# Kernel tuning notes

Hardware: AMD Instinct MI355X
Metric: run time of the kernel (lower is better)

Reference implementation:

```python
import jax, jax.numpy as jnp
import numpy as np

B, S, D, H, F = 2, 1024, 2048, 16, 8192
DH = D // H
MAX_ALPHA = 0.2
CN_SCALE = D / (D - 1)  # CenterNorm scale factor dim/(dim-1)


def setup_inputs() -> dict:
    key = jax.random.key(0)
    ks = jax.random.split(key, 8)
    s = 0.02
    f32 = jnp.float32
    return {
        "x": jax.random.normal(ks[0], (B, S, D), f32),
        "ln1_g": jnp.ones((D,), f32), "ln1_b": jnp.zeros((D,), f32),
        "wq": jax.random.normal(ks[1], (D, D), f32) * s, "bq": jnp.zeros((D,), f32),
        "wk": jax.random.normal(ks[2], (D, D), f32) * s, "bk": jnp.zeros((D,), f32),
        "wv": jax.random.normal(ks[3], (D, D), f32) * s, "bv": jnp.zeros((D,), f32),
        "wo": jax.random.normal(ks[4], (D, D), f32) * s, "bo": jnp.zeros((D,), f32),
        "tau": jnp.ones((H,), f32),   # learnable per-head temperature, init_tau=1.0
        "nu": jnp.ones((H,), f32),    # learnable per-head output scale, init_nu=1.0
        "alpha1": jnp.full((D,), 0.1, f32),  # per-channel residual weight, init 0.1
        "ln2_g": jnp.ones((D,), f32), "ln2_b": jnp.zeros((D,), f32),
        "w1": jax.random.normal(ks[5], (F, D), f32) * s, "b1": jnp.zeros((F,), f32),
        "w2": jax.random.normal(ks[6], (D, F), f32) * s, "b2": jnp.zeros((D,), f32),
        "alpha2": jnp.full((D,), 0.1, f32),
    }


def _center_norm(x, g, b):
    # CenterNorm: subtract mean only (no variance), scale by dim/(dim-1)
    mu = jnp.mean(x, axis=-1, keepdims=True)
    return g * (CN_SCALE * (x - mu)) + b


def _l2norm(t):
    return t / (jnp.linalg.norm(t, axis=-1, keepdims=True) + 1e-6)


def _cosine_attn(x, wq, bq, wk, bk, wv, bv, wo, bo, tau, nu):
    # project and split heads -> [B,H,S,DH]
    def proj(w, b):
        return (jnp.einsum('bsd,ed->bse', x, w) + b).reshape(B, S, H, DH).transpose(0, 2, 1, 3)
    q, k, v = proj(wq, bq), proj(wk, bk), proj(wv, bv)
    qn, kn = _l2norm(q), _l2norm(k)  # cosine similarity attention
    scores = jnp.einsum('bhqd,bhkd->bhqk', qn, kn) * tau[None, :, None, None]
    causal = jnp.tril(jnp.ones((S, S), bool))
    scores = jnp.where(causal[None, None], scores, -jnp.inf)
    p = jax.nn.softmax(scores, axis=-1)
    o = jnp.einsum('bhqk,bhkd->bhqd', p, v) * nu[None, :, None, None]
    o = o.transpose(0, 2, 1, 3).reshape(B, S, D)
    return jnp.einsum('bsd,ed->bse', o, wo) + bo


def _ffn(x, w1, b1, w2, b2):
    h = jax.nn.gelu(jnp.einsum('bsd,fd->bsf', x, w1) + b1)
    return jnp.einsum('bsf,df->bsd', h, w2) + b2


def reference(x, ln1_g, ln1_b, wq, bq, wk, bk, wv, bv, wo, bo, tau, nu,
              alpha1, ln2_g, ln2_b, w1, b1, w2, b2, alpha2):
    a = _center_norm(x, ln1_g, ln1_b)
    a1 = jnp.clip(alpha1, -MAX_ALPHA, MAX_ALPHA)
    x1 = a + a1 * _cosine_attn(a, wq, bq, wk, bk, wv, bv, wo, bo, tau, nu)
    m = _center_norm(x1, ln2_g, ln2_b)
    a2 = jnp.clip(alpha2, -MAX_ALPHA, MAX_ALPHA)
    return m + a2 * _ffn(m, w1, b1, w2, b2)
```

## Files before the change

### kernel.cpp

```cpp
#include <hip/hip_runtime.h>
#include <hip/hip_bf16.h>
#include <stdint.h>

#define B_ 2
#define S_ 1024
#define D_ 2048
#define H_ 16
#define F_ 8192
#define DH_ 128
#define M_ 2048

typedef unsigned short u16;
typedef __attribute__((ext_vector_type(8))) short short8;
typedef __attribute__((ext_vector_type(4))) float f32x4;
typedef __attribute__((ext_vector_type(2))) float f32x2;

__device__ __forceinline__ u16 f2bf(float f) {
  union { float f; uint32_t u; } c; c.f = f;
  uint32_t r = c.u + 0x7FFFu + ((c.u >> 16) & 1u);
  return (u16)(r >> 16);
}

__device__ __forceinline__ float bf2f(u16 v) {
  union { uint32_t u; float f; } c; c.u = ((uint32_t)v) << 16;
  return c.f;
}

__device__ __forceinline__ void gload16(const void* g, void* l) {
  __builtin_amdgcn_global_load_lds((const __attribute__((address_space(1))) void*)g,
                                   (__attribute__((address_space(3))) void*)l, 16, 0, 0);
}

__device__ __forceinline__ float clipa(float a) {
  return fminf(0.2f, fmaxf(-0.2f, a));
}

__device__ __forceinline__ float gelu_f(float x) {
  float z = 0.7978845608028654f * (x + 0.044715f * x * x * x);
  z = fminf(10.f, fmaxf(-10.f, z));
  float e = __expf(2.f * z);
  return 0.5f * x * (1.f + (e - 1.f) / (e + 1.f));
}

__global__ __launch_bounds__(256) void k_cvt_all(const float* __restrict__ wq,
                                                 const float* __restrict__ wk,
                                                 const float* __restrict__ wv,
                                                 const float* __restrict__ wo,
                                                 const float* __restrict__ w1,
                                                 const float* __restrict__ w2,
                                                 u16* __restrict__ dst) {
  const int tot = 6291456;
  for (int gi = blockIdx.x * 256 + threadIdx.x; gi < tot; gi += 2048 * 256) {
    const float* s;
    int off;
    if (gi < 2097152) {
      int r = gi >> 19;
      s = r == 0 ? wq : (r == 1 ? wk : (r == 2 ? wv : wo));
      off = gi & 524287;
    } else if (gi < 4194304) {
      s = w1; off = gi - 2097152;
    } else {
      s = w2; off = gi - 4194304;
    }
    f32x4 a = *(const f32x4*)(s + (size_t)off * 8);
    f32x4 b = *(const f32x4*)(s + (size_t)off * 8 + 4);
    short8 o;
    o[0] = (short)f2bf(a[0]); o[1] = (short)f2bf(a[1]);
    o[2] = (short)f2bf(a[2]); o[3] = (short)f2bf(a[3]);
    o[4] = (short)f2bf(b[0]); o[5] = (short)f2bf(b[1]);
    o[6] = (short)f2bf(b[2]); o[7] = (short)f2bf(b[3]);
    *(short8*)(dst + (size_t)gi * 8) = o;
  }
}

__global__ __launch_bounds__(256) void k_centernorm(const float* __restrict__ x,
                                                    const float* __restrict__ g,
                                                    const float* __restrict__ bb,
                                                    float* __restrict__ of,
                                                    u16* __restrict__ ob) {
  const int row = blockIdx.x;
  const int t = threadIdx.x;
  const float* xr = x + (size_t)row * D_;
  f32x4 v0 = *(const f32x4*)(xr + t * 8);
  f32x4 v1 = *(const f32x4*)(xr + t * 8 + 4);
  float s = v0[0] + v0[1] + v0[2] + v0[3] + v1[0] + v1[1] + v1[2] + v1[3];
#pragma unroll
  for (int off = 1; off < 64; off <<= 1) s += __shfl_xor(s, off);
  __shared__ float red[4];
  if ((t & 63) == 0) red[t >> 6] = s;
  __syncthreads();
  const float mu = (red[0] + red[1] + red[2] + red[3]) * (1.0f / D_);
  const float CNS = (float)D_ / (float)(D_ - 1);
  f32x4 g0 = *(const f32x4*)(g + t * 8);
  f32x4 g1 = *(const f32x4*)(g + t * 8 + 4);
  f32x4 b0 = *(const f32x4*)(bb + t * 8);
  f32x4 b1 = *(const f32x4*)(bb + t * 8 + 4);
  f32x4 y0, y1;
  short8 yb;
#pragma unroll
  for (int i = 0; i < 4; i++) {
    y0[i] = g0[i] * (CNS * (v0[i] - mu)) + b0[i];
    y1[i] = g1[i] * (CNS * (v1[i] - mu)) + b1[i];
  }
#pragma unroll
  for (int i = 0; i < 4; i++) { yb[i] = (short)f2bf(y0[i]); yb[4 + i] = (short)f2bf(y1[i]); }
  float* orow = of + (size_t)row * D_;
  *(f32x4*)(orow + t * 8) = y0;
  *(f32x4*)(orow + t * 8 + 4) = y1;
  *(short8*)(ob + (size_t)row * D_ + t * 8) = yb;
}

template <int EPI>
__device__ __forceinline__ void gemm256_core(const u16* __restrict__ A,
                                             const u16* __restrict__ Bt,
                                             const float* __restrict__ bias,
                                             float* __restrict__ outf,
                                             u16* __restrict__ outb,
                                             int N, int K, int kbase, int nk,
                                             int m0, int n0,
                                             const float* __restrict__ tau,
                                             u16* __restrict__ qkv, int z) {
  __shared__ char lds[2][65536];
  const int t = threadIdx.x;
  const int l = t & 63, w = t >> 6;
  const int wr = w >> 2, wc = w & 3;
  const int l15 = l & 15, lhi = l >> 4;
  const int sw = (l15 & 7) << 4;
  const int ab0 = l15 * 128 + ((lhi * 16) ^ sw);
  const int ab1 = l15 * 128 + ((64 + lhi * 16) ^ sw);

  auto stage = [&](int kt, int h) {
#pragma unroll
    for (int rj = 0; rj < 4; rj++) {
      const int region = rj >> 1, j = rj & 1;
      const int pl = h * 16384 + j * 8192 + t * 16;
      const int row = pl >> 7;
      const int scol = (pl & 127) ^ ((row & 7) << 4);
      const int grow = (region ? n0 : m0) + row;
      const char* src = (const char*)(region ? Bt : A) +
                        (size_t)grow * (size_t)(K * 2) +
                        (size_t)((kbase + kt * 64) * 2 + scol);
      gload16(src, &lds[kt & 1][region * 32768 + pl]);
    }
  };

  f32x4 acc[8][4] = {};

  stage(0, 0); stage(0, 1); stage(1, 0);
  asm volatile("s_waitcnt vmcnt(4)" ::: "memory");
  __builtin_amdgcn_s_barrier();
  __builtin_amdgcn_sched_barrier(0);

  for (int kt = 0; kt < nk; ++kt) {
    const char* base = &lds[kt & 1][0];
    const char* pA0 = base + wr * 4096 + ab0;
    const char* pA1 = base + wr * 4096 + ab1;
    const char* pB0 = base + 32768 + wc * 8192 + ab0;
    const char* pB1 = base + 32768 + wc * 8192 + ab1;
    short8 bf[4][2];
#pragma unroll
    for (int ni = 0; ni < 4; ni++) {
      bf[ni][0] = *(const short8*)(pB0 + ni * 2048);
      bf[ni][1] = *(const short8*)(pB1 + ni * 2048);
    }
#pragma unroll
    for (int q = 0; q < 4; q++) {
      short8 aq[2][2];
#pragma unroll
      for (int mi = 0; mi < 2; mi++) {
        aq[mi][0] = *(const short8*)(pA0 + q * 8192 + mi * 2048);
        aq[mi][1] = *(const short8*)(pA1 + q * 8192 + mi * 2048);
      }
      if (q == 1 && kt + 1 < nk) stage(kt + 1, 1);
      if (q == 3 && kt + 2 < nk) stage(kt + 2, 0);
      __builtin_amdgcn_s_setprio(1);
#pragma unroll
      for (int ks = 0; ks < 2; ks++)
#pragma unroll
        for (int mi = 0; mi < 2; mi++)
#pragma unroll
          for (int ni = 0; ni < 4; ni++)
            acc[q * 2 + mi][ni] = __builtin_amdgcn_mfma_f32_16x16x32_bf16(
                aq[mi][ks], bf[ni][ks], acc[q * 2 + mi][ni], 0, 0, 0);
      __builtin_amdgcn_s_setprio(0);
      if (q == 1) __builtin_amdgcn_s_barrier();
    }
    if (kt + 1 < nk) {
      if (kt + 2 < nk) { asm volatile("s_waitcnt vmcnt(4)" ::: "memory"); }
      else             { asm volatile("s_waitcnt vmcnt(0)" ::: "memory"); }
      __builtin_amdgcn_s_barrier();
      __builtin_amdgcn_sched_barrier(0);
    }
  }

  if constexpr (EPI == 4) {
    __shared__ float part[4][256];
#pragma unroll
    for (int ni = 0; ni < 4; ni++) {
      const float bc = bias[n0 + wc * 64 + ni * 16 + l15];
#pragma unroll
      for (int ai = 0; ai < 8; ai++)
#pragma unroll
        for (int j = 0; j < 4; j++) acc[ai][ni][j] += bc;
    }
    if (z < 2) {
      float p[8][4];
#pragma unroll
      for (int ai = 0; ai < 8; ai++)
#pragma unroll
        for (int j = 0; j < 4; j++) {
          p[ai][j] = acc[ai][0][j] * acc[ai][0][j] + acc[ai][1][j] * acc[ai][1][j] +
                     acc[ai][2][j] * acc[ai][2][j] + acc[ai][3][j] * acc[ai][3][j];
#pragma unroll
          for (int off = 1; off < 16; off <<= 1) p[ai][j] += __shfl_xor(p[ai][j], off);
        }
      if (l15 == 0) {
#pragma unroll
        for (int ai = 0; ai < 8; ai++)
#pragma unroll
          for (int j = 0; j < 4; j++) {
            const int rb = (ai >> 1) * 64 + wr * 32 + (ai & 1) * 16 + lhi * 4 + j;
            part[wc][rb] = p[ai][j];
          }
      }
    }
    __syncthreads();
    const int hl = wc >> 1;
    const int hglob = (n0 >> 7) + hl;
    const float tauh = (z == 0) ? tau[hglob] : 1.f;
    char* yt = (char*)&lds[0][0] + w * 16384;
#pragma unroll
    for (int ai = 0; ai < 8; ai++) {
#pragma unroll
      for (int j = 0; j < 4; j++) {
        float sc = 1.f;
        if (z < 2) {
          const int rb = (ai >> 1) * 64 + wr * 32 + (ai & 1) * 16 + lhi * 4 + j;
          const float ssq = part[2 * hl][rb] + part[2 * hl + 1][rb];
          sc = tauh / (sqrtf(ssq) + 1e-6f);
        }
        const int rl = (ai >> 1) * 32 + (ai & 1) * 16 + lhi * 4 + j;
        const int swz = (rl & 7) << 4;
#pragma unroll
        for (int ni = 0; ni < 4; ni++) {
          const int cbyte = (ni * 16 + l15) * 2;
          *(u16*)(yt + rl * 128 + (cbyte ^ swz)) = f2bf(acc[ai][ni][j] * sc);
        }
      }
    }
    __syncthreads();
#pragma unroll
    for (int pass = 0; pass < 16; pass++) {
      const int rl = pass * 8 + (l >> 3);
      const int cb = (l & 7) * 16;
      const short8 v = *(const short8*)(yt + rl * 128 + (cb ^ ((rl & 7) << 4)));
      const int m = m0 + ((rl >> 5) << 6) + wr * 32 + (rl & 31);
      const int bb2 = m >> 10, s = m & 1023;
      const int d = (wc & 1) * 64 + (cb >> 1);
      *(short8*)(qkv + (((size_t)(bb2 * H_ + hglob)) * S_ + s) * DH_ + d) = v;
    }
    return;
  }

#pragma unroll
  for (int ni = 0; ni < 4; ni++) {
    const int col = n0 + wc * 64 + ni * 16 + l15;
    const float bcol = (EPI == 3) ? 0.f : bias[col];
#pragma unroll
    for (int ai = 0; ai < 8; ai++) {
      const int row = m0 + (ai >> 1) * 64 + wr * 32 + (ai & 1) * 16 + lhi * 4;
#pragma unroll
      for (int j = 0; j < 4; j++) {
        const float v = acc[ai][ni][j] + bcol;
        const size_t idx = (size_t)(row + j) * N + col;
        if (EPI == 0) outf[idx] = v;
        else if (EPI == 2) outb[idx] = f2bf(gelu_f(v));
        else outb[idx] = f2bf(v);
      }
    }
  }
}

__global__ __launch_bounds__(512, 2) void k_qkv256(const u16* A, const u16* W,
                                                   const float* b0, const float* b1,
                                                   const float* b2, const float* tau,
                                                   u16* qn, u16* kn, u16* vn) {
  const int z = blockIdx.z;
  const u16* Bt = W + (size_t)z * 4194304;
  const float* bias = z == 0 ? b0 : (z == 1 ? b1 : b2);
  u16* dst = z == 0 ? qn : (z == 1 ? kn : vn);
  gemm256_core<4>(A, Bt, bias, nullptr, nullptr, D_, D_, 0, 32,
                  blockIdx.y * 256, blockIdx.x * 256, tau, dst, z);
}

__global__ __launch_bounds__(512, 2) void k_ffn1_256(const u16* A, const u16* Bt,
                                                     const float* bias, u16* outb) {
  gemm256_core<2>(A, Bt, bias, nullptr, outb, F_, D_, 0, 32,
                  blockIdx.y * 256, blockIdx.x * 256, nullptr, nullptr, 0);
}

__global__ __launch_bounds__(512, 2) void k_ffn2_256(const u16* A, const u16* Bt, u16* P) {
  gemm256_core<3>(A, Bt, nullptr, nullptr, P + (size_t)blockIdx.z * M_ * D_, D_, F_,
                  blockIdx.z * 2048, 32, blockIdx.y * 256, blockIdx.x * 256,
                  nullptr, nullptr, 0);
}

__device__ __forceinline__ void gemm128_res(const u16* __restrict__ A,
                                            const u16* __restrict__ Bt,
                                            const float* __restrict__ bias,
                                            const float* __restrict__ res,
                                            const float* __restrict__ alpha,
                                            float* __restrict__ outf, int N, int K) {
  __shared__ u16 As[2][128 * 32];
  __shared__ u16 Bs[2][128 * 32];
  const int t = threadIdx.x;
  const int l = t & 63;
  const int w = t >> 6;
  const int wr = w >> 1, wc = w & 1;
  const int l15 = l & 15, lhi = l >> 4;
  const int m0 = blockIdx.y * 128, n0 = blockIdx.x * 128;
  f32x4 acc[4][4] = {};
  const int srow = t >> 2;
  const int scol = (t & 3) * 8;
  const u16* Ag = A + (size_t)(m0 + srow) * K + scol;
  const u16* Ag2 = Ag + (size_t)64 * K;
  const u16* Bg = Bt + (size_t)(n0 + srow) * K + scol;
  const u16* Bg2 = Bg + (size_t)64 * K;
  const int loff = t * 16;
  const int kiters = K / 32;

  gload16(Ag, (char*)As[0] + loff);
  gload16(Ag2, (char*)As[0] + 4096 + loff);
  gload16(Bg, (char*)Bs[0] + loff);
  gload16(Bg2, (char*)Bs[0] + 4096 + loff);
  __syncthreads();

  int cur = 0;
  for (int it = 0; it < kiters; ++it) {
    if (it + 1 < kiters) {
      const int k0 = (it + 1) * 32;
      char* dA = (char*)As[cur ^ 1] + loff;
      char* dB = (char*)Bs[cur ^ 1] + loff;
      gload16(Ag + k0, dA);
      gload16(Ag2 + k0, dA + 4096);
      gload16(Bg + k0, dB);
      gload16(Bg2 + k0, dB + 4096);
    }
    short8 af[4], bfr[4];
#pragma unroll
    for (int i = 0; i < 4; i++)
      af[i] = *(const short8*)(As[cur] + (wr * 64 + i * 16 + l15) * 32 + lhi * 8);
#pragma unroll
    for (int i = 0; i < 4; i++)
      bfr[i] = *(const short8*)(Bs[cur] + (wc * 64 + i * 16 + l15) * 32 + lhi * 8);
#pragma unroll
    for (int mi = 0; mi < 4; mi++)
#pragma unroll
      for (int ni = 0; ni < 4; ni++)
        acc[mi][ni] = __builtin_amdgcn_mfma_f32_16x16x32_bf16(af[mi], bfr[ni], acc[mi][ni], 0, 0, 0);
    __syncthreads();
    cur ^= 1;
  }
#pragma unroll
  for (int ni = 0; ni < 4; ni++) {
    const int col = n0 + wc * 64 + ni * 16 + l15;
    const float bcol = bias[col];
    const float alc = clipa(alpha[col]);
#pragma unroll
    for (int mi = 0; mi < 4; mi++) {
#pragma unroll
      for (int j = 0; j < 4; j++) {
        const int row = m0 + wr * 64 + mi * 16 + lhi * 4 + j;
        const size_t idx = (size_t)row * N + col;
        outf[idx] = res[idx] + alc * (acc[mi][ni][j] + bcol);
      }
    }
  }
}

__global__ __launch_bounds__(256) void k_oproj(const u16* A, const u16* Bt, const float* bias,
                                               const float* res, const float* alpha,
                                               float* outf) {
  gemm128_res(A, Bt, bias, res, alpha, outf, D_, D_);
}

__global__ __launch_bounds__(256) void k_ffn2_combine(const u16* __restrict__ P,
                                                      const float* __restrict__ bias,
                                                      const float* __restrict__ res,
                                                      const float* __restrict__ alpha,
                                                      float* __restrict__ out) {
  const int i = blockIdx.x * 256 + threadIdx.x;
  const size_t base = (size_t)i * 8;
  const int col = (int)(base & (D_ - 1));
  const size_t PS = (size_t)M_ * D_;
  float s[8] = {};
#pragma unroll
  for (int p = 0; p < 4; p++) {
    short8 v = *(const short8*)(P + p * PS + base);
#pragma unroll
    for (int j = 0; j < 8; j++) s[j] += bf2f((u16)v[j]);
  }
  f32x4 b0 = *(const f32x4*)(bias + col);
  f32x4 b1 = *(const f32x4*)(bias + col + 4);
  f32x4 a0 = *(const f32x4*)(alpha + col);
  f32x4 a1 = *(const f32x4*)(alpha + col + 4);
  f32x4 r0 = *(const f32x4*)(res + base);
  f32x4 r1 = *(const f32x4*)(res + base + 4);
  f32x4 o0, o1;
#pragma unroll
  for (int j = 0; j < 4; j++) {
    o0[j] = r0[j] + clipa(a0[j]) * (s[j] + b0[j]);
    o1[j] = r1[j] + clipa(a1[j]) * (s[4 + j] + b1[j]);
  }
  *(f32x4*)(out + base) = o0;
  *(f32x4*)(out + base + 4) = o1;
}

__global__ __launch_bounds__(256) void k_attn(const u16* __restrict__ qn,
                                              const u16* __restrict__ kn,
                                              const u16* __restrict__ vn,
                                              const float* __restrict__ nu,
                                              u16* __restrict__ o) {
  __shared__ u16 Ks[64 * 128];
  __shared__ u16 Vt[128 * 64];
  __shared__ u16 Pl[4][16][72];
  const int t = threadIdx.x;
  const int l = t & 63, w = t >> 6;
  const int l15 = l & 15, lhi = l >> 4;
  const int qt = blockIdx.x;
  const int bh = blockIdx.y;
  const int h = bh & (H_ - 1);
  const int b = bh >> 4;
  const size_t hoff = (size_t)bh * S_ * DH_;
  const u16* Qh = qn + hoff;
  const u16* Kh = kn + hoff;
  const u16* Vh = vn + hoff;
  const int q0 = qt * 64;
  const int r0 = q0 + w * 16;
  short8 qf[4];
#pragma unroll
  for (int kk = 0; kk < 4; kk++)
    qf[kk] = *(const short8*)(Qh + (size_t)(r0 + l15) * DH_ + kk * 32 + lhi * 8);
  float mrow[4], lrow[4];
  f32x4 oacc[8] = {};
#pragma unroll
  for (int j = 0; j < 4; j++) { mrow[j] = -1e30f; lrow[j] = 0.f; }

  for (int kv0 = 0; kv0 < q0 + 64; kv0 += 64) {
#pragma unroll
    for (int i = 0; i < 4; i++) {
      const int p = i * 4096 + t * 16;
      const int row = p >> 8;
      const int colb = p & 255;
      const int scolb = colb ^ ((row & 7) << 4);
      gload16((const char*)(Kh + (size_t)(kv0 + row) * DH_) + scolb, (char*)Ks + p);
    }
#pragma unroll
    for (int i = 0; i < 4; i++) {
      const int c0 = w * 8 + i * 32;
      const int r = l;
      short8 vv = *(const short8*)(Vh + (size_t)(kv0 + r) * DH_ + c0);
#pragma unroll
      for (int j = 0; j < 8; j++) {
        const int ba = ((c0 + j) * 128 + r * 2) ^ (((c0 + j) & 7) << 4);
        *(u16*)((char*)Vt + ba) = (u16)vv[j];
      }
    }
    __syncthreads();
    f32x4 st[4] = {};
#pragma unroll
    for (int ks = 0; ks < 4; ks++) {
#pragma unroll
      for (int ct = 0; ct < 4; ct++) {
        const int n = ct * 16 + l15;
        const int ka = (ks * 32 + lhi * 8) * 2;
        short8 kf = *(const short8*)((const char*)Ks + n * 256 + (ka ^ ((n & 7) << 4)));
        st[ct] = __builtin_amdgcn_mfma_f32_16x16x32_bf16(qf[ks], kf, st[ct], 0, 0, 0);
      }
    }
    float pm[4] = {-1e30f, -1e30f, -1e30f, -1e30f};
#pragma unroll
    for (int ct = 0; ct < 4; ct++) {
      const int col = kv0 + ct * 16 + l15;
#pragma unroll
      for (int j = 0; j < 4; j++) {
        const int row = r0 + lhi * 4 + j;
        float s = st[ct][j];
        s = (col <= row) ? s : -1e30f;
        st[ct][j] = s;
        pm[j] = fmaxf(pm[j], s);
      }
    }
#pragma unroll
    for (int j = 0; j < 4; j++) {
#pragma unroll
      for (int off = 1; off < 16; off <<= 1) pm[j] = fmaxf(pm[j], __shfl_xor(pm[j], off));
    }
    float scl[4], psum[4];
#pragma unroll
    for (int j = 0; j < 4; j++) {
      const float nm = fmaxf(mrow[j], pm[j]);
      scl[j] = __expf(mrow[j] - nm);
      mrow[j] = nm;
      psum[j] = 0.f;
    }
#pragma unroll
    for (int ct = 0; ct < 4; ct++) {
#pragma unroll
      for (int j = 0; j < 4; j++) {
        const float p = __expf(st[ct][j] - mrow[j]);
        psum[j] += p;
        Pl[w][lhi * 4 + j][ct * 16 + l15] = f2bf(p);
      }
    }
#pragma unroll
    for (int j = 0; j < 4; j++) {
#pragma unroll
      for (int off = 1; off < 16; off <<= 1) psum[j] += __shfl_xor(psum[j], off);
      lrow[j] = lrow[j] * scl[j] + psum[j];
    }
#pragma unroll
    for (int nt = 0; nt < 8; nt++) {
#pragma unroll
      for (int j = 0; j < 4; j++) oacc[nt][j] *= scl[j];
    }
#pragma unroll
    for (int ks2 = 0; ks2 < 2; ks2++) {
      short8 pa = *(const short8*)((const char*)&Pl[w][0][0] + l15 * 144 + ks2 * 64 + lhi * 16);
#pragma unroll
      for (int nt = 0; nt < 8; nt++) {
        const int n = nt * 16 + l15;
        const int ba = (n * 128 + (ks2 * 32 + lhi * 8) * 2) ^ ((n & 7) << 4);
        short8 vf = *(const short8*)((const char*)Vt + ba);
        oacc[nt] = __builtin_amdgcn_mfma_f32_16x16x32_bf16(pa, vf, oacc[nt], 0, 0, 0);
      }
    }
    __syncthreads();
  }
  const float num = nu[h];
  float rs[4];
#pragma unroll
  for (int j = 0; j < 4; j++) rs[j] = num / lrow[j];
#pragma unroll
  for (int nt = 0; nt < 8; nt++) {
    const int col = h * DH_ + nt * 16 + l15;
#pragma unroll
    for (int j = 0; j < 4; j++) {
      const int row = r0 + lhi * 4 + j;
      o[((size_t)b * S_ + row) * D_ + col] = f2bf(oacc[nt][j] * rs[j]);
    }
  }
}

extern "C" void kernel_launch(void* const* d_in, const int* in_sizes, int n_in,
                              void* d_out, int out_size, void* d_ws, size_t ws_size,
                              hipStream_t stream) {
  const float* x    = (const float*)d_in[0];
  const float* ln1g = (const float*)d_in[1];
  const float* ln1b = (const float*)d_in[2];
  const float* wq   = (const float*)d_in[3];
  const float* bq   = (const float*)d_in[4];
  const float* wk   = (const float*)d_in[5];
  const float* bk   = (const float*)d_in[6];
  const float* wv   = (const float*)d_in[7];
  const float* bv   = (const float*)d_in[8];
  const float* wo   = (const float*)d_in[9];
  const float* bo   = (const float*)d_in[10];
  const float* tau  = (const float*)d_in[11];
  const float* nu   = (const float*)d_in[12];
  const float* al1  = (const float*)d_in[13];
  const float* ln2g = (const float*)d_in[14];
  const float* ln2b = (const float*)d_in[15];
  const float* w1   = (const float*)d_in[16];
  const float* b1   = (const float*)d_in[17];
  const float* w2   = (const float*)d_in[18];
  const float* b2   = (const float*)d_in[19];
  const float* al2  = (const float*)d_in[20];

  char* ws = (char*)d_ws;
  u16* WQ = (u16*)(ws + 0);
  u16* WO = (u16*)(ws + 25165824);
  u16* W1B = (u16*)(ws + 33554432);
  u16* W2B = (u16*)(ws + 67108864);
  float* AF = (float*)(ws + 100663296);
  u16*   AB = (u16*)(ws + 117440512);
  u16*   OB = (u16*)(ws + 125829120);
  u16*   MB = (u16*)(ws + 134217728);
  float* X1 = (float*)(ws + 142606336);
  float* MF2 = (float*)(ws + 159383552);
  u16* QN = (u16*)(ws + 176160768);
  u16* KN = (u16*)(ws + 184549376);
  u16* VN = (u16*)(ws + 192937984);
  u16*   HB = (u16*)(ws + 176160768);
  u16*   P4 = (u16*)(ws + 0);

  k_cvt_all<<<2048, 256, 0, stream>>>(wq, wk, wv, wo, w1, w2, WQ);

  k_centernorm<<<M_, 256, 0, stream>>>(x, ln1g, ln1b, AF, AB);

  k_qkv256<<<dim3(8, 8, 3), 512, 0, stream>>>(AB, WQ, bq, bk, bv, tau, QN, KN, VN);

  k_attn<<<dim3(S_ / 64, B_ * H_), 256, 0, stream>>>(QN, KN, VN, nu, OB);

  k_oproj<<<dim3(16, 16), 256, 0, stream>>>(OB, WO, bo, AF, al1, X1);

  k_centernorm<<<M_, 256, 0, stream>>>(X1, ln2g, ln2b, MF2, MB);

  k_ffn1_256<<<dim3(32, 8), 512, 0, stream>>>(MB, W1B, b1, HB);

  k_ffn2_256<<<dim3(8, 8, 4), 512, 0, stream>>>(HB, W2B, P4);
  k_ffn2_combine<<<2048, 256, 0, stream>>>(P4, b2, MF2, al2, (float*)d_out);
}
```

Measured before the change: 409.1 us.

## Rewrite o-proj GEMM with swizzled 128-wide K tiles and split-stage pipelining; split weight cast

The output-projection GEMM now stages 64-element K tiles into an XOR-swizzled LDS layout. Each tile is split into two halves loaded at different points of the loop, with explicit vmcnt waits, barriers and setprio around the MFMA groups. The aim is to overlap global loads with compute and reduce LDS bank conflicts, with two blocks per CU. The weight-conversion kernel becomes one thread per 8 elements with no grid-stride loop, launched twice over halves of the data, which drops the loop overhead but adds an extra launch.

```diff
diff --git a/kernel.cpp b/kernel.cpp
--- a/kernel.cpp
+++ b/kernel.cpp
@@ -42,35 +42,33 @@
   return 0.5f * x * (1.f + (e - 1.f) / (e + 1.f));
 }
 
-__global__ __launch_bounds__(256) void k_cvt_all(const float* __restrict__ wq,
-                                                 const float* __restrict__ wk,
-                                                 const float* __restrict__ wv,
-                                                 const float* __restrict__ wo,
-                                                 const float* __restrict__ w1,
-                                                 const float* __restrict__ w2,
-                                                 u16* __restrict__ dst) {
-  const int tot = 6291456;
-  for (int gi = blockIdx.x * 256 + threadIdx.x; gi < tot; gi += 2048 * 256) {
-    const float* s;
-    int off;
-    if (gi < 2097152) {
-      int r = gi >> 19;
-      s = r == 0 ? wq : (r == 1 ? wk : (r == 2 ? wv : wo));
-      off = gi & 524287;
-    } else if (gi < 4194304) {
-      s = w1; off = gi - 2097152;
-    } else {
-      s = w2; off = gi - 4194304;
-    }
-    f32x4 a = *(const f32x4*)(s + (size_t)off * 8);
-    f32x4 b = *(const f32x4*)(s + (size_t)off * 8 + 4);
-    short8 o;
-    o[0] = (short)f2bf(a[0]); o[1] = (short)f2bf(a[1]);
-    o[2] = (short)f2bf(a[2]); o[3] = (short)f2bf(a[3]);
-    o[4] = (short)f2bf(b[0]); o[5] = (short)f2bf(b[1]);
-    o[6] = (short)f2bf(b[2]); o[7] = (short)f2bf(b[3]);
-    *(short8*)(dst + (size_t)gi * 8) = o;
-  }
+__global__ __launch_bounds__(256) void k_cvt_half(const float* __restrict__ wq,
+                                                  const float* __restrict__ wk,
+                                                  const float* __restrict__ wv,
+                                                  const float* __restrict__ wo,
+                                                  const float* __restrict__ w1,
+                                                  const float* __restrict__ w2,
+                                                  u16* __restrict__ dst, int base) {
+  const int gi = base + blockIdx.x * 256 + threadIdx.x;
+  const float* s;
+  int off;
+  if (gi < 2097152) {
+    int r = gi >> 19;
+    s = r == 0 ? wq : (r == 1 ? wk : (r == 2 ? wv : wo));
+    off = gi & 524287;
+  } else if (gi < 4194304) {
+    s = w1; off = gi - 2097152;
+  } else {
+    s = w2; off = gi - 4194304;
+  }
+  f32x4 a = *(const f32x4*)(s + (size_t)off * 8);
+  f32x4 b = *(const f32x4*)(s + (size_t)off * 8 + 4);
+  short8 o;
+  o[0] = (short)f2bf(a[0]); o[1] = (short)f2bf(a[1]);
+  o[2] = (short)f2bf(a[2]); o[3] = (short)f2bf(a[3]);
+  o[4] = (short)f2bf(b[0]); o[5] = (short)f2bf(b[1]);
+  o[6] = (short)f2bf(b[2]); o[7] = (short)f2bf(b[3]);
+  *(short8*)(dst + (size_t)gi * 8) = o;
 }
 
 __global__ __launch_bounds__(256) void k_centernorm(const float* __restrict__ x,
@@ -305,83 +303,98 @@
                   nullptr, nullptr, 0);
 }
 
-__device__ __forceinline__ void gemm128_res(const u16* __restrict__ A,
-                                            const u16* __restrict__ Bt,
-                                            const float* __restrict__ bias,
-                                            const float* __restrict__ res,
-                                            const float* __restrict__ alpha,
-                                            float* __restrict__ outf, int N, int K) {
-  __shared__ u16 As[2][128 * 32];
-  __shared__ u16 Bs[2][128 * 32];
+__global__ __launch_bounds__(256, 2) void k_oproj(const u16* __restrict__ A,
+                                                  const u16* __restrict__ Bt,
+                                                  const float* __restrict__ bias,
+                                                  const float* __restrict__ res,
+                                                  const float* __restrict__ alpha,
+                                                  float* __restrict__ outf) {
+  const int N = D_, K = D_, nk = 32;
+  const int m0 = blockIdx.y * 128, n0 = blockIdx.x * 128;
+  __shared__ char lds[2][32768];
   const int t = threadIdx.x;
-  const int l = t & 63;
-  const int w = t >> 6;
+  const int l = t & 63, w = t >> 6;
   const int wr = w >> 1, wc = w & 1;
   const int l15 = l & 15, lhi = l >> 4;
-  const int m0 = blockIdx.y * 128, n0 = blockIdx.x * 128;
+  const int sw = (l15 & 7) << 4;
+  const int ab0 = l15 * 128 + ((lhi * 16) ^ sw);
+  const int ab1 = l15 * 128 + ((64 + lhi * 16) ^ sw);
+
+  auto stage = [&](int kt, int h) {
+#pragma unroll
+    for (int rj = 0; rj < 4; rj++) {
+      const int region = rj >> 1, j = rj & 1;
+      const int pl = h * 8192 + j * 4096 + t * 16;
+      const int row = pl >> 7;
+      const int scol = (pl & 127) ^ ((row & 7) << 4);
+      const int grow = (region ? n0 : m0) + row;
+      const char* src = (const char*)(region ? Bt : A) +
+                        (size_t)grow * (size_t)(K * 2) + (size_t)(kt * 128 + scol);
+      gload16(src, &lds[kt & 1][region * 16384 + pl]);
+    }
+  };
+
   f32x4 acc[4][4] = {};
-  const int srow = t >> 2;
-  const int scol = (t & 3) * 8;
-  const u16* Ag = A + (size_t)(m0 + srow) * K + scol;
-  const u16* Ag2 = Ag + (size_t)64 * K;
-  const u16* Bg = Bt + (size_t)(n0 + srow) * K + scol;
-  const u16* Bg2 = Bg + (size_t)64 * K;
-  const int loff = t * 16;
-  const int kiters = K / 32;
-
-  gload16(Ag, (char*)As[0] + loff);
-  gload16(Ag2, (char*)As[0] + 4096 + loff);
-  gload16(Bg, (char*)Bs[0] + loff);
-  gload16(Bg2, (char*)Bs[0] + 4096 + loff);
-  __syncthreads();
-
-  int cur = 0;
-  for (int it = 0; it < kiters; ++it) {
-    if (it + 1 < kiters) {
-      const int k0 = (it + 1) * 32;
-      char* dA = (char*)As[cur ^ 1] + loff;
-      char* dB = (char*)Bs[cur ^ 1] + loff;
-      gload16(Ag + k0, dA);
-      gload16(Ag2 + k0, dA + 4096);
-      gload16(Bg + k0, dB);
-      gload16(Bg2 + k0, dB + 4096);
-    }
-    short8 af[4], bfr[4];
-#pragma unroll
-    for (int i = 0; i < 4; i++)
-      af[i] = *(const short8*)(As[cur] + (wr * 64 + i * 16 + l15) * 32 + lhi * 8);
-#pragma unroll
-    for (int i = 0; i < 4; i++)
-      bfr[i] = *(const short8*)(Bs[cur] + (wc * 64 + i * 16 + l15) * 32 + lhi * 8);
-#pragma unroll
-    for (int mi = 0; mi < 4; mi++)
-#pragma unroll
-      for (int ni = 0; ni < 4; ni++)
-        acc[mi][ni] = __builtin_amdgcn_mfma_f32_16x16x32_bf16(af[mi], bfr[ni], acc[mi][ni], 0, 0, 0);
-    __syncthreads();
-    cur ^= 1;
-  }
+  stage(0, 0); stage(0, 1); stage(1, 0);
+  asm volatile("s_waitcnt vmcnt(4)" ::: "memory");
+  __builtin_amdgcn_s_barrier();
+  __builtin_amdgcn_sched_barrier(0);
+
+  for (int kt = 0; kt < nk; ++kt) {
+    const char* base = &lds[kt & 1][0];
+    const char* pB0 = base + 16384 + wc * 8192 + ab0;
+    const char* pB1 = base + 16384 + wc * 8192 + ab1;
+    short8 bf[4][2];
+#pragma unroll
+    for (int ni = 0; ni < 4; ni++) {
+      bf[ni][0] = *(const short8*)(pB0 + ni * 2048);
+      bf[ni][1] = *(const short8*)(pB1 + ni * 2048);
+    }
+#pragma unroll
+    for (int q = 0; q < 2; q++) {
+      short8 aq[2][2];
+#pragma unroll
+      for (int mi = 0; mi < 2; mi++) {
+        aq[mi][0] = *(const short8*)(base + q * 8192 + wr * 4096 + mi * 2048 + ab0);
+        aq[mi][1] = *(const short8*)(base + q * 8192 + wr * 4096 + mi * 2048 + ab1);
+      }
+      if (q == 0 && kt + 1 < nk) stage(kt + 1, 1);
+      if (q == 1 && kt + 2 < nk) stage(kt + 2, 0);
+      __builtin_amdgcn_s_setprio(1);
+#pragma unroll
+      for (int ks = 0; ks < 2; ks++)
+#pragma unroll
+        for (int mi = 0; mi < 2; mi++)
+#pragma unroll
+          for (int ni = 0; ni < 4; ni++)
+            acc[q * 2 + mi][ni] = __builtin_amdgcn_mfma_f32_16x16x32_bf16(
+                aq[mi][ks], bf[ni][ks], acc[q * 2 + mi][ni], 0, 0, 0);
+      __builtin_amdgcn_s_setprio(0);
+      if (q == 0) __builtin_amdgcn_s_barrier();
+    }
+    if (kt + 1 < nk) {
+      if (kt + 2 < nk) { asm volatile("s_waitcnt vmcnt(4)" ::: "memory"); }
+      else             { asm volatile("s_waitcnt vmcnt(0)" ::: "memory"); }
+      __builtin_amdgcn_s_barrier();
+      __builtin_amdgcn_sched_barrier(0);
+    }
+  }
+
 #pragma unroll
   for (int ni = 0; ni < 4; ni++) {
     const int col = n0 + wc * 64 + ni * 16 + l15;
     const float bcol = bias[col];
     const float alc = clipa(alpha[col]);
 #pragma unroll
-    for (int mi = 0; mi < 4; mi++) {
+    for (int ai = 0; ai < 4; ai++) {
+      const int row = m0 + (ai >> 1) * 64 + wr * 32 + (ai & 1) * 16 + lhi * 4;
 #pragma unroll
       for (int j = 0; j < 4; j++) {
-        const int row = m0 + wr * 64 + mi * 16 + lhi * 4 + j;
-        const size_t idx = (size_t)row * N + col;
-        outf[idx] = res[idx] + alc * (acc[mi][ni][j] + bcol);
-      }
-    }
-  }
-}
-
-__global__ __launch_bounds__(256) void k_oproj(const u16* A, const u16* Bt, const float* bias,
-                                               const float* res, const float* alpha,
-                                               float* outf) {
-  gemm128_res(A, Bt, bias, res, alpha, outf, D_, D_);
+        const size_t idx = (size_t)(row + j) * N + col;
+        outf[idx] = res[idx] + alc * (acc[ai][ni][j] + bcol);
+      }
+    }
+  }
 }
 
 __global__ __launch_bounds__(256) void k_ffn2_combine(const u16* __restrict__ P,
@@ -594,7 +607,8 @@
   u16*   HB = (u16*)(ws + 176160768);
   u16*   P4 = (u16*)(ws + 0);
 
-  k_cvt_all<<<2048, 256, 0, stream>>>(wq, wk, wv, wo, w1, w2, WQ);
+  k_cvt_half<<<12288, 256, 0, stream>>>(wq, wk, wv, wo, w1, w2, WQ, 0);
+  k_cvt_half<<<12288, 256, 0, stream>>>(wq, wk, wv, wo, w1, w2, WQ, 3145728);
 
   k_centernorm<<<M_, 256, 0, stream>>>(x, ln1g, ln1b, AF, AB);
 
```

Result: faster. 372.5 us (-8.9%).
